# Kernel optimization log

Measured on AMD Instinct MI355X. Metric: run time of the kernel, lower is better.

## Reference

```python
import jax, jax.numpy as jnp
import numpy as np

H = 1024
BATCH, T = 16, 2048

def setup_inputs() -> dict:
    key = jax.random.key(0)
    k1, k2, k3, k4 = jax.random.split(key, 4)
    scale = 1.0 / (H ** 0.5)
    return {
        "u_sequence": jax.random.normal(k1, (BATCH, T, 1), dtype=jnp.float32),
        "A": jax.random.normal(k2, (H, H), dtype=jnp.float32) * scale,
        "B": jax.random.normal(k3, (H, 1), dtype=jnp.float32) * scale,
        "C": jax.random.normal(k4, (1, H), dtype=jnp.float32) * scale,
        "D": jnp.zeros((1,), dtype=jnp.float32),
    }

def reference(u_sequence, A, B, C, D):
    # u_sequence: [Bt, T, 1]
    u = u_sequence[..., 0]            # [Bt, T]
    b_vec = B[:, 0]                   # [H]

    def step(h, u_t):
        # h: [Bt, H], u_t: [Bt]
        h_new = h @ A.T + u_t[:, None] * b_vec[None, :]
        return h_new, h_new

    h0 = jnp.zeros((u.shape[0], H), dtype=u.dtype)
    _, h_stack = jax.lax.scan(step, h0, u.T)   # h_stack: [T, Bt, H]
    h_stack = jnp.swapaxes(h_stack, 0, 1)      # [Bt, T, H]
    y = jnp.einsum("bth,h->bt", h_stack, C[0]) + u * D[0]
    return y[..., None]                         # [Bt, T, 1]
```

## Files before the change

### kernel.cpp

```cpp
#include <hip/hip_runtime.h>

#define HDIM 1024
#define TLEN 2048
#define NBATCH 16

typedef short bf16x8 __attribute__((ext_vector_type(8)));
typedef float floatx4 __attribute__((ext_vector_type(4)));
typedef unsigned short ushort_t;

__device__ __forceinline__ ushort_t f2bf(float x) {
  unsigned u = __float_as_uint(x);
  unsigned r = (u + 0x7FFFu + ((u >> 16) & 1u)) >> 16;
  return (ushort_t)r;
}
__device__ __forceinline__ float bf2f(ushort_t h) {
  return __uint_as_float(((unsigned)h) << 16);
}

typedef __attribute__((address_space(1))) void gvoid_t;
typedef __attribute__((address_space(3))) void lvoid_t;
__device__ __forceinline__ void gload16(const ushort_t* g, ushort_t* l) {
  __builtin_amdgcn_global_load_lds((gvoid_t*)g, (lvoid_t*)l, 16, 0, 0);
}

template <int N>
__device__ __forceinline__ void vmwait() {
  if constexpr (N == 0) asm volatile("s_waitcnt vmcnt(0)" ::: "memory");
  else if constexpr (N == 4) asm volatile("s_waitcnt vmcnt(4)" ::: "memory");
  else asm volatile("s_waitcnt vmcnt(6)" ::: "memory");
}
__device__ __forceinline__ void phase_barrier() {
  __builtin_amdgcn_sched_barrier(0);
  __builtin_amdgcn_s_barrier();
  __builtin_amdgcn_sched_barrier(0);
  asm volatile("" ::: "memory");
}

#define TSTR 71

__global__ __launch_bounds__(256) void prep(const float* __restrict__ A,
    const float* __restrict__ Bv, const float* __restrict__ Cv,
    ushort_t* __restrict__ Ah, ushort_t* __restrict__ Am, ushort_t* __restrict__ Al,
    ushort_t* __restrict__ ATh, ushort_t* __restrict__ ATm, ushort_t* __restrict__ ATl,
    float* __restrict__ Vc, float* __restrict__ U) {
  __shared__ ushort_t Lt[3 * 64 * TSTR];
  const int tid = threadIdx.x;
  if (blockIdx.x >= 256) {
    int i = (blockIdx.x - 256) * 256 + tid;
    if (i < HDIM) Vc[i] = Bv[i];
    else U[i - HDIM] = Cv[i - HDIM];
    return;
  }
  const int row0 = (blockIdx.x >> 4) * 64, col0 = (blockIdx.x & 15) * 64;
  const int r = tid >> 2, q = tid & 3;
  ushort_t hs[16], ms[16], ls[16];
#pragma unroll
  for (int c4 = 0; c4 < 4; ++c4) {
    float4 a = *(const float4*)&A[(row0 + r) * HDIM + col0 + q * 16 + c4 * 4];
    float av[4] = {a.x, a.y, a.z, a.w};
#pragma unroll
    for (int i = 0; i < 4; ++i) {
      float z = av[i];
      ushort_t h = f2bf(z); float r1 = z - bf2f(h);
      ushort_t mq = f2bf(r1); float r2 = r1 - bf2f(mq);
      ushort_t lq = f2bf(r2);
      hs[c4 * 4 + i] = h; ms[c4 * 4 + i] = mq; ls[c4 * 4 + i] = lq;
    }
  }
  size_t go = (size_t)(row0 + r) * HDIM + col0 + q * 16;
  *(uint4*)&Ah[go] = ((uint4*)hs)[0]; *(uint4*)&Ah[go + 8] = ((uint4*)hs)[1];
  *(uint4*)&Am[go] = ((uint4*)ms)[0]; *(uint4*)&Am[go + 8] = ((uint4*)ms)[1];
  *(uint4*)&Al[go] = ((uint4*)ls)[0]; *(uint4*)&Al[go + 8] = ((uint4*)ls)[1];
#pragma unroll
  for (int i = 0; i < 16; ++i) {
    int c = q * 16 + i;
    Lt[0 * 64 * TSTR + r * TSTR + c] = hs[i];
    Lt[1 * 64 * TSTR + r * TSTR + c] = ms[i];
    Lt[2 * 64 * TSTR + r * TSTR + c] = ls[i];
  }
  __syncthreads();
  const int c = tid >> 2, q2 = tid & 3;
  ushort_t* dsts[3] = {ATh, ATm, ATl};
#pragma unroll
  for (int s = 0; s < 3; ++s) {
    ushort_t tmp[16];
#pragma unroll
    for (int rr = 0; rr < 16; ++rr) tmp[rr] = Lt[s * 64 * TSTR + (q2 * 16 + rr) * TSTR + c];
    size_t gt = (size_t)(col0 + c) * HDIM + row0 + q2 * 16;
    *(uint4*)&dsts[s][gt] = ((uint4*)tmp)[0];
    *(uint4*)&dsts[s][gt + 8] = ((uint4*)tmp)[1];
  }
}

template <int MODE, int NC, bool SIX, bool WRITEL, bool WROW>
__global__ __launch_bounds__(256) void sq_mfma(
    const ushort_t* __restrict__ Xh, const ushort_t* __restrict__ Xm,
    const ushort_t* __restrict__ Xl,
    const ushort_t* __restrict__ XTh, const ushort_t* __restrict__ XTm,
    const ushort_t* __restrict__ XTl,
    ushort_t* __restrict__ Zh, ushort_t* __restrict__ Zm, ushort_t* __restrict__ Zl,
    ushort_t* __restrict__ ZTh, ushort_t* __restrict__ ZTm, ushort_t* __restrict__ ZTl,
    const float* __restrict__ Af, const float* __restrict__ Bvf,
    float* __restrict__ VU) {
  constexpr int NARR = SIX ? 6 : 4;
  constexpr int SLAB = 64 * 32;
  constexpr int BUFSTR = NARR * SLAB;
  constexpr int BBASE = (SIX ? 3 : 2) * SLAB;
  constexpr int LDS_ELEMS = 3 * BUFSTR;
  __shared__ __align__(16) ushort_t sm[LDS_ELEMS];
  const int tid = threadIdx.x;

  if (blockIdx.x >= 256) {
    const int tb = blockIdx.x - 256;
    const int wv = tb * 4 + (tid >> 6);
    const int lane = tid & 63;
    if (MODE == 0) {
      float acc = 0.f;
      for (int k = lane; k < HDIM; k += 64) acc += Af[(size_t)wv * HDIM + k] * Bvf[k];
      for (int off = 32; off; off >>= 1) acc += __shfl_down(acc, off);
      if (lane == 0) VU[HDIM + wv] = acc;
    } else {
      const ushort_t* Ph = (MODE == 1) ? Xh : XTh;
      const ushort_t* Pm = (MODE == 1) ? Xm : XTm;
      float acc[NC];
#pragma unroll
      for (int n = 0; n < NC; ++n) acc[n] = 0.f;
      for (int k = lane; k < HDIM; k += 64) {
        float a = bf2f(Ph[(size_t)wv * HDIM + k]) + bf2f(Pm[(size_t)wv * HDIM + k]);
#pragma unroll
        for (int n = 0; n < NC; ++n) acc[n] += a * VU[(size_t)n * HDIM + k];
      }
#pragma unroll
      for (int n = 0; n < NC; ++n) {
        float s = acc[n];
        for (int off = 32; off; off >>= 1) s += __shfl_down(s, off);
        if (lane == 0) VU[(size_t)(NC + n) * HDIM + wv] = s;
      }
    }
    return;
  }

  const int bb = blockIdx.x;
  const int xcd = bb & 7, slot = bb >> 3;
  const int tr = 4 * (xcd >> 1) + (slot >> 3);
  const int tc = 8 * (xcd & 1) + (slot & 7);
  const int row0 = tr * 64, col0 = tc * 64;

  const int w = tid >> 6, l = tid & 63, li = l & 15, quad = l >> 4;
  const int sr = tid >> 2, sq4 = tid & 3;

  floatx4 acc0 = {0.f, 0.f, 0.f, 0.f}, acc1 = acc0, acc2 = acc0, acc3 = acc0;

  const int aoff = (w * 16 + li) * 32 + quad * 8;
  const int b0o = (0 * 16 + li) * 32 + quad * 8;
  const int b1o = (1 * 16 + li) * 32 + quad * 8;
  const int b2o = (2 * 16 + li) * 32 + quad * 8;
  const int b3o = (3 * 16 + li) * 32 + quad * 8;

  const ushort_t* gAh = Xh + (size_t)(row0 + sr) * HDIM + sq4 * 8;
  const ushort_t* gAm = Xm + (size_t)(row0 + sr) * HDIM + sq4 * 8;
  const ushort_t* gAl = Xl + (size_t)(row0 + sr) * HDIM + sq4 * 8;
  const ushort_t* gBh = XTh + (size_t)(col0 + sr) * HDIM + sq4 * 8;
  const ushort_t* gBm = XTm + (size_t)(col0 + sr) * HDIM + sq4 * 8;
  const ushort_t* gBl = XTl + (size_t)(col0 + sr) * HDIM + sq4 * 8;

  ushort_t* lwb = &sm[w * 512];

#define STAGE(BUF, K)                                                          \
  {                                                                            \
    ushort_t* lb = lwb + (BUF) * BUFSTR;                                       \
    const int kk = (K);                                                        \
    gload16(gAh + kk, lb);                                                     \
    gload16(gAm + kk, lb + SLAB);                                              \
    if (SIX) gload16(gAl + kk, lb + 2 * SLAB);                                 \
    gload16(gBh + kk, lb + BBASE);                                             \
    gload16(gBm + kk, lb + BBASE + SLAB);                                      \
    if (SIX) gload16(gBl + kk, lb + BBASE + 2 * SLAB);                         \
  }

  STAGE(0, 0)
  STAGE(1, 32)
  vmwait<NARR>();
  phase_barrier();

  int cur = 0, nx2 = 2;
  for (int k0 = 0; k0 < HDIM; k0 += 32) {
    if (k0 + 64 < HDIM) STAGE(nx2, k0 + 64)
    const int cb = cur * BUFSTR;
    bf16x8 ah = *(const bf16x8*)&sm[cb + aoff];
    bf16x8 am = *(const bf16x8*)&sm[cb + SLAB + aoff];
    bf16x8 al;
    if (SIX) al = *(const bf16x8*)&sm[cb + 2 * SLAB + aoff];
    {
      bf16x8 bh = *(const bf16x8*)&sm[cb + BBASE + b0o];
      bf16x8 bm = *(const bf16x8*)&sm[cb + BBASE + SLAB + b0o];
      acc0 = __builtin_amdgcn_mfma_f32_16x16x32_bf16(ah, bh, acc0, 0, 0, 0);
      acc0 = __builtin_amdgcn_mfma_f32_16x16x32_bf16(ah, bm, acc0, 0, 0, 0);
      acc0 = __builtin_amdgcn_mfma_f32_16x16x32_bf16(am, bh, acc0, 0, 0, 0);
      acc0 = __builtin_amdgcn_mfma_f32_16x16x32_bf16(am, bm, acc0, 0, 0, 0);
      if (SIX) {
        bf16x8 bl = *(const bf16x8*)&sm[cb + BBASE + 2 * SLAB + b0o];
        acc0 = __builtin_amdgcn_mfma_f32_16x16x32_bf16(ah, bl, acc0, 0, 0, 0);
        acc0 = __builtin_amdgcn_mfma_f32_16x16x32_bf16(al, bh, acc0, 0, 0, 0);
      }
    }
    {
      bf16x8 bh = *(const bf16x8*)&sm[cb + BBASE + b1o];
      bf16x8 bm = *(const bf16x8*)&sm[cb + BBASE + SLAB + b1o];
      acc1 = __builtin_amdgcn_mfma_f32_16x16x32_bf16(ah, bh, acc1, 0, 0, 0);
      acc1 = __builtin_amdgcn_mfma_f32_16x16x32_bf16(ah, bm, acc1, 0, 0, 0);
      acc1 = __builtin_amdgcn_mfma_f32_16x16x32_bf16(am, bh, acc1, 0, 0, 0);
      acc1 = __builtin_amdgcn_mfma_f32_16x16x32_bf16(am, bm, acc1, 0, 0, 0);
      if (SIX) {
        bf16x8 bl = *(const bf16x8*)&sm[cb + BBASE + 2 * SLAB + b1o];
        acc1 = __builtin_amdgcn_mfma_f32_16x16x32_bf16(ah, bl, acc1, 0, 0, 0);
        acc1 = __builtin_amdgcn_mfma_f32_16x16x32_bf16(al, bh, acc1, 0, 0, 0);
      }
    }
    {
      bf16x8 bh = *(const bf16x8*)&sm[cb + BBASE + b2o];
      bf16x8 bm = *(const bf16x8*)&sm[cb + BBASE + SLAB + b2o];
      acc2 = __builtin_amdgcn_mfma_f32_16x16x32_bf16(ah, bh, acc2, 0, 0, 0);
      acc2 = __builtin_amdgcn_mfma_f32_16x16x32_bf16(ah, bm, acc2, 0, 0, 0);
      acc2 = __builtin_amdgcn_mfma_f32_16x16x32_bf16(am, bh, acc2, 0, 0, 0);
      acc2 = __builtin_amdgcn_mfma_f32_16x16x32_bf16(am, bm, acc2, 0, 0, 0);
      if (SIX) {
        bf16x8 bl = *(const bf16x8*)&sm[cb + BBASE + 2 * SLAB + b2o];
        acc2 = __builtin_amdgcn_mfma_f32_16x16x32_bf16(ah, bl, acc2, 0, 0, 0);
        acc2 = __builtin_amdgcn_mfma_f32_16x16x32_bf16(al, bh, acc2, 0, 0, 0);
      }
    }
    {
      bf16x8 bh = *(const bf16x8*)&sm[cb + BBASE + b3o];
      bf16x8 bm = *(const bf16x8*)&sm[cb + BBASE + SLAB + b3o];
      acc3 = __builtin_amdgcn_mfma_f32_16x16x32_bf16(ah, bh, acc3, 0, 0, 0);
      acc3 = __builtin_amdgcn_mfma_f32_16x16x32_bf16(ah, bm, acc3, 0, 0, 0);
      acc3 = __builtin_amdgcn_mfma_f32_16x16x32_bf16(am, bh, acc3, 0, 0, 0);
      acc3 = __builtin_amdgcn_mfma_f32_16x16x32_bf16(am, bm, acc3, 0, 0, 0);
      if (SIX) {
        bf16x8 bl = *(const bf16x8*)&sm[cb + BBASE + 2 * SLAB + b3o];
        acc3 = __builtin_amdgcn_mfma_f32_16x16x32_bf16(ah, bl, acc3, 0, 0, 0);
        acc3 = __builtin_amdgcn_mfma_f32_16x16x32_bf16(al, bh, acc3, 0, 0, 0);
      }
    }
    asm volatile("" ::: "memory");
    if (k0 + 64 < HDIM) vmwait<NARR>(); else vmwait<0>();
    phase_barrier();
    cur = (cur == 2) ? 0 : cur + 1;
    nx2 = (nx2 == 2) ? 0 : nx2 + 1;
  }
#undef STAGE

  floatx4 accs[4] = {acc0, acc1, acc2, acc3};
#pragma unroll
  for (int j = 0; j < 4; ++j) {
#pragma unroll
    for (int e = 0; e < 4; ++e) {
      float z = accs[j][e];
      int rl = w * 16 + quad * 4 + e;
      int cl = j * 16 + li;
      size_t go = (size_t)(row0 + rl) * HDIM + col0 + cl;
      ushort_t h = f2bf(z); float r1 = z - bf2f(h);
      ushort_t mq = f2bf(r1);
      if (WROW) { Zh[go] = h; Zm[go] = mq; }
      sm[0 * 64 * TSTR + rl * TSTR + cl] = h;
      sm[1 * 64 * TSTR + rl * TSTR + cl] = mq;
      if (WRITEL) {
        ushort_t lq = f2bf(r1 - bf2f(mq));
        if (WROW) Zl[go] = lq;
        sm[2 * 64 * TSTR + rl * TSTR + cl] = lq;
      }
    }
  }
  __syncthreads();
  const int c = tid >> 2, q2 = tid & 3;
  ushort_t* dsts[3] = {ZTh, ZTm, ZTl};
  const int npass = WRITEL ? 3 : 2;
#pragma unroll
  for (int s = 0; s < 3; ++s) {
    if (s >= npass) break;
    ushort_t tmp[16];
#pragma unroll
    for (int rr = 0; rr < 16; ++rr) tmp[rr] = sm[s * 64 * TSTR + (q2 * 16 + rr) * TSTR + c];
    size_t gt = (size_t)(col0 + c) * HDIM + row0 + q2 * 16;
    *(uint4*)&dsts[s][gt] = ((uint4*)tmp)[0];
    *(uint4*)&dsts[s][gt + 8] = ((uint4*)tmp)[1];
  }
}

__global__ __launch_bounds__(256) void utail8(const ushort_t* __restrict__ PTh,
                                              const ushort_t* __restrict__ PTm,
                                              float* __restrict__ U, int dstbase) {
  const int wv = blockIdx.x * 4 + (threadIdx.x >> 6);
  const int lane = threadIdx.x & 63;
  float acc[8];
#pragma unroll
  for (int m = 0; m < 8; ++m) acc[m] = 0.f;
  const float* Usrc = U + (size_t)(dstbase - 8) * HDIM;
  for (int k = lane; k < HDIM; k += 64) {
    float a = bf2f(PTh[(size_t)wv * HDIM + k]) + bf2f(PTm[(size_t)wv * HDIM + k]);
#pragma unroll
    for (int m = 0; m < 8; ++m) acc[m] += a * Usrc[(size_t)m * HDIM + k];
  }
#pragma unroll
  for (int m = 0; m < 8; ++m) {
    float s = acc[m];
    for (int off = 32; off; off >>= 1) s += __shfl_down(s, off);
    if (lane == 0) U[(size_t)(dstbase + m) * HDIM + wv] = s;
  }
}

__global__ __launch_bounds__(256) void wavedotK(const float* __restrict__ U,
                                                const float* __restrict__ Vc,
                                                float* __restrict__ Km) {
  int wv = (blockIdx.x * blockDim.x + threadIdx.x) >> 6;
  int lane = threadIdx.x & 63;
  if (wv >= 32 * 64) return;
  int mr = wv >> 6;
  int nc = wv & 63;
  float s = 0.f;
  for (int k = lane; k < HDIM; k += 64) s += U[mr * HDIM + k] * Vc[nc * HDIM + k];
  for (int off = 32; off; off >>= 1) s += __shfl_down(s, off);
  if (lane == 0) Km[wv] = s;
}

__global__ __launch_bounds__(256) void convk2(const float* __restrict__ u,
                                              const float* __restrict__ Km,
                                              const float* __restrict__ Dv,
                                              float* __restrict__ y) {
  __shared__ float ks[256];
  __shared__ float us[512];
  const int tt = threadIdx.x;
  const int t0 = blockIdx.x * 256;
  const int b = blockIdx.y;
  const float* ub = u + (size_t)b * TLEN;
  const int t = t0 + tt;
  float s0 = Dv[0] * ub[t], s1 = 0.f, s2 = 0.f, s3 = 0.f;
  for (int mc = 0; mc <= t0; mc += 256) {
    __syncthreads();
    ks[tt] = Km[mc + tt];
    int w0 = t0 - mc - 255;
    int g0 = w0 + tt;
    us[tt] = (g0 >= 0) ? ub[g0] : 0.f;
    int g1 = w0 + 256 + tt;
    us[256 + tt] = (g1 < TLEN) ? ub[g1] : 0.f;
    __syncthreads();
    if (mc < t0) {
#pragma unroll 4
      for (int r = 0; r < 256; r += 4) {
        float4 kv = *(const float4*)&ks[r];
        s0 += kv.x * us[tt - r + 255];
        s1 += kv.y * us[tt - r + 254];
        s2 += kv.z * us[tt - r + 253];
        s3 += kv.w * us[tt - r + 252];
      }
    } else {
      for (int r = 0; r <= tt; ++r) s0 += ks[r] * us[tt - r + 255];
    }
  }
  y[(size_t)b * TLEN + t] = s0 + s1 + s2 + s3;
}

extern "C" void kernel_launch(void* const* d_in, const int* in_sizes, int n_in,
                              void* d_out, int out_size, void* d_ws, size_t ws_size,
                              hipStream_t stream) {
  const float* u  = (const float*)d_in[0];
  const float* A  = (const float*)d_in[1];
  const float* Bv = (const float*)d_in[2];
  const float* Cv = (const float*)d_in[3];
  const float* Dv = (const float*)d_in[4];
  float* out = (float*)d_out;

  char* wsb = (char*)d_ws;
  size_t off = 0;
  ushort_t* S[2][6];
  for (int s = 0; s < 2; ++s)
    for (int a = 0; a < 6; ++a) { S[s][a] = (ushort_t*)(wsb + off); off += (size_t)2 << 20; }
  float* Vc = (float*)(wsb + off); off += 64 * HDIM * 4;
  float* U  = (float*)(wsb + off); off += 32 * HDIM * 4;
  float* Km = (float*)(wsb + off); off += TLEN * 4;

  const dim3 gsq(512);

#define SQ(MODE, NC, SIX, WRL, WROW, IN, OUT, VU)                              \
  sq_mfma<MODE, NC, SIX, WRL, WROW><<<gsq, 256, 0, stream>>>(                  \
      S[IN][0], S[IN][1], S[IN][2], S[IN][3], S[IN][4], S[IN][5],              \
      S[OUT][0], S[OUT][1], S[OUT][2], S[OUT][3], S[OUT][4], S[OUT][5],        \
      A, Bv, VU)

  prep<<<dim3(264), 256, 0, stream>>>(A, Bv, Cv,
      S[0][0], S[0][1], S[0][2], S[0][3], S[0][4], S[0][5], Vc, U);

  SQ(0, 1,  true,  true,  true,  0, 1, Vc);
  SQ(1, 2,  true,  true,  true,  1, 0, Vc);
  SQ(1, 4,  true,  true,  true,  0, 1, Vc);
  SQ(1, 8,  true,  false, true,  1, 0, Vc);
  SQ(1, 16, false, false, true,  0, 1, Vc);
  SQ(1, 32, false, false, true,  1, 0, Vc);
  SQ(2, 1,  false, false, true,  0, 1, U);
  SQ(2, 2,  false, false, true,  1, 0, U);
  SQ(2, 4,  false, false, false, 0, 1, U);
#undef SQ

  utail8<<<dim3(256), 256, 0, stream>>>(S[1][3], S[1][4], U, 8);
  utail8<<<dim3(256), 256, 0, stream>>>(S[1][3], S[1][4], U, 16);
  utail8<<<dim3(256), 256, 0, stream>>>(S[1][3], S[1][4], U, 24);

  wavedotK<<<dim3(512), 256, 0, stream>>>(U, Vc, Km);
  convk2<<<dim3(TLEN / 256, NBATCH), 256, 0, stream>>>(u, Km, Dv, out);
}
```

Measured before the change: 301.9 us.

## Use 512-thread blocks with 2x4 wave grid in squaring GEMM kernel

The squaring MFMA kernel moves from 4 waves per 64x64 tile (each wave computing 16x64) to 8 waves (each computing 16x32), so blocks have 512 threads. Only the first 256 threads issue the global-to-LDS loads, and the transposed writeback is re-split across 512 threads. The matvec tail blocks now use 8 waves each, so the grid shrinks to 384 blocks. The goal is more waves per tile to hide MFMA and LDS latency, at the cost of redundant A-fragment LDS reads across waves and fewer accumulators per wave.

```diff
diff --git a/kernel.cpp b/kernel.cpp
--- a/kernel.cpp
+++ b/kernel.cpp
@@ -93,7 +93,7 @@
 }
 
 template <int MODE, int NC, bool SIX, bool WRITEL, bool WROW>
-__global__ __launch_bounds__(256) void sq_mfma(
+__global__ __launch_bounds__(512) void sq_mfma(
     const ushort_t* __restrict__ Xh, const ushort_t* __restrict__ Xm,
     const ushort_t* __restrict__ Xl,
     const ushort_t* __restrict__ XTh, const ushort_t* __restrict__ XTm,
@@ -112,7 +112,7 @@
 
   if (blockIdx.x >= 256) {
     const int tb = blockIdx.x - 256;
-    const int wv = tb * 4 + (tid >> 6);
+    const int wv = tb * 8 + (tid >> 6);
     const int lane = tid & 63;
     if (MODE == 0) {
       float acc = 0.f;
@@ -147,15 +147,14 @@
   const int row0 = tr * 64, col0 = tc * 64;
 
   const int w = tid >> 6, l = tid & 63, li = l & 15, quad = l >> 4;
-  const int sr = tid >> 2, sq4 = tid & 3;
-
-  floatx4 acc0 = {0.f, 0.f, 0.f, 0.f}, acc1 = acc0, acc2 = acc0, acc3 = acc0;
-
-  const int aoff = (w * 16 + li) * 32 + quad * 8;
-  const int b0o = (0 * 16 + li) * 32 + quad * 8;
-  const int b1o = (1 * 16 + li) * 32 + quad * 8;
-  const int b2o = (2 * 16 + li) * 32 + quad * 8;
-  const int b3o = (3 * 16 + li) * 32 + quad * 8;
+  const int wr = w >> 1, wc = w & 1;
+  const int sr = (tid & 255) >> 2, sq4 = tid & 3;
+
+  floatx4 acc0 = {0.f, 0.f, 0.f, 0.f}, acc1 = acc0;
+
+  const int aoff = (wr * 16 + li) * 32 + quad * 8;
+  const int b0o = (wc * 32 + li) * 32 + quad * 8;
+  const int b1o = (wc * 32 + 16 + li) * 32 + quad * 8;
 
   const ushort_t* gAh = Xh + (size_t)(row0 + sr) * HDIM + sq4 * 8;
   const ushort_t* gAm = Xm + (size_t)(row0 + sr) * HDIM + sq4 * 8;
@@ -178,14 +177,16 @@
     if (SIX) gload16(gBl + kk, lb + BBASE + 2 * SLAB);                         \
   }
 
-  STAGE(0, 0)
-  STAGE(1, 32)
+  if (tid < 256) {
+    STAGE(0, 0)
+    STAGE(1, 32)
+  }
   vmwait<NARR>();
   phase_barrier();
 
   int cur = 0, nx2 = 2;
   for (int k0 = 0; k0 < HDIM; k0 += 32) {
-    if (k0 + 64 < HDIM) STAGE(nx2, k0 + 64)
+    if (tid < 256 && k0 + 64 < HDIM) STAGE(nx2, k0 + 64)
     const int cb = cur * BUFSTR;
     bf16x8 ah = *(const bf16x8*)&sm[cb + aoff];
     bf16x8 am = *(const bf16x8*)&sm[cb + SLAB + aoff];
@@ -217,32 +218,6 @@
         acc1 = __builtin_amdgcn_mfma_f32_16x16x32_bf16(al, bh, acc1, 0, 0, 0);
       }
     }
-    {
-      bf16x8 bh = *(const bf16x8*)&sm[cb + BBASE + b2o];
-      bf16x8 bm = *(const bf16x8*)&sm[cb + BBASE + SLAB + b2o];
-      acc2 = __builtin_amdgcn_mfma_f32_16x16x32_bf16(ah, bh, acc2, 0, 0, 0);
-      acc2 = __builtin_amdgcn_mfma_f32_16x16x32_bf16(ah, bm, acc2, 0, 0, 0);
-      acc2 = __builtin_amdgcn_mfma_f32_16x16x32_bf16(am, bh, acc2, 0, 0, 0);
-      acc2 = __builtin_amdgcn_mfma_f32_16x16x32_bf16(am, bm, acc2, 0, 0, 0);
-      if (SIX) {
-        bf16x8 bl = *(const bf16x8*)&sm[cb + BBASE + 2 * SLAB + b2o];
-        acc2 = __builtin_amdgcn_mfma_f32_16x16x32_bf16(ah, bl, acc2, 0, 0, 0);
-        acc2 = __builtin_amdgcn_mfma_f32_16x16x32_bf16(al, bh, acc2, 0, 0, 0);
-      }
-    }
-    {
-      bf16x8 bh = *(const bf16x8*)&sm[cb + BBASE + b3o];
-      bf16x8 bm = *(const bf16x8*)&sm[cb + BBASE + SLAB + b3o];
-      acc3 = __builtin_amdgcn_mfma_f32_16x16x32_bf16(ah, bh, acc3, 0, 0, 0);
-      acc3 = __builtin_amdgcn_mfma_f32_16x16x32_bf16(ah, bm, acc3, 0, 0, 0);
-      acc3 = __builtin_amdgcn_mfma_f32_16x16x32_bf16(am, bh, acc3, 0, 0, 0);
-      acc3 = __builtin_amdgcn_mfma_f32_16x16x32_bf16(am, bm, acc3, 0, 0, 0);
-      if (SIX) {
-        bf16x8 bl = *(const bf16x8*)&sm[cb + BBASE + 2 * SLAB + b3o];
-        acc3 = __builtin_amdgcn_mfma_f32_16x16x32_bf16(ah, bl, acc3, 0, 0, 0);
-        acc3 = __builtin_amdgcn_mfma_f32_16x16x32_bf16(al, bh, acc3, 0, 0, 0);
-      }
-    }
     asm volatile("" ::: "memory");
     if (k0 + 64 < HDIM) vmwait<NARR>(); else vmwait<0>();
     phase_barrier();
@@ -251,14 +226,14 @@
   }
 #undef STAGE
 
-  floatx4 accs[4] = {acc0, acc1, acc2, acc3};
-#pragma unroll
-  for (int j = 0; j < 4; ++j) {
+  floatx4 accs[2] = {acc0, acc1};
+#pragma unroll
+  for (int j = 0; j < 2; ++j) {
 #pragma unroll
     for (int e = 0; e < 4; ++e) {
       float z = accs[j][e];
-      int rl = w * 16 + quad * 4 + e;
-      int cl = j * 16 + li;
+      int rl = wr * 16 + quad * 4 + e;
+      int cl = wc * 32 + j * 16 + li;
       size_t go = (size_t)(row0 + rl) * HDIM + col0 + cl;
       ushort_t h = f2bf(z); float r1 = z - bf2f(h);
       ushort_t mq = f2bf(r1);
@@ -273,18 +248,17 @@
     }
   }
   __syncthreads();
-  const int c = tid >> 2, q2 = tid & 3;
+  const int c = tid >> 3, q3 = tid & 7;
   ushort_t* dsts[3] = {ZTh, ZTm, ZTl};
   const int npass = WRITEL ? 3 : 2;
 #pragma unroll
   for (int s = 0; s < 3; ++s) {
     if (s >= npass) break;
-    ushort_t tmp[16];
-#pragma unroll
-    for (int rr = 0; rr < 16; ++rr) tmp[rr] = sm[s * 64 * TSTR + (q2 * 16 + rr) * TSTR + c];
-    size_t gt = (size_t)(col0 + c) * HDIM + row0 + q2 * 16;
-    *(uint4*)&dsts[s][gt] = ((uint4*)tmp)[0];
-    *(uint4*)&dsts[s][gt + 8] = ((uint4*)tmp)[1];
+    ushort_t tmp[8];
+#pragma unroll
+    for (int rr = 0; rr < 8; ++rr) tmp[rr] = sm[s * 64 * TSTR + (q3 * 8 + rr) * TSTR + c];
+    size_t gt = (size_t)(col0 + c) * HDIM + row0 + q3 * 8;
+    *(uint4*)&dsts[s][gt] = *(uint4*)tmp;
   }
 }
 
@@ -380,10 +354,10 @@
   float* U  = (float*)(wsb + off); off += 32 * HDIM * 4;
   float* Km = (float*)(wsb + off); off += TLEN * 4;
 
-  const dim3 gsq(512);
+  const dim3 gsq(384);
 
 #define SQ(MODE, NC, SIX, WRL, WROW, IN, OUT, VU)                              \
-  sq_mfma<MODE, NC, SIX, WRL, WROW><<<gsq, 256, 0, stream>>>(                  \
+  sq_mfma<MODE, NC, SIX, WRL, WROW><<<gsq, 512, 0, stream>>>(                  \
       S[IN][0], S[IN][1], S[IN][2], S[IN][3], S[IN][4], S[IN][5],              \
       S[OUT][0], S[OUT][1], S[OUT][2], S[OUT][3], S[OUT][4], S[OUT][5],        \
       A, Bv, VU)
```

Result: no change. 299.7 us (-0.8%).
